# Kernel optimization log

Measured on AMD Instinct MI355X. Metric: run time of the kernel, lower is better.

## Reference

```python
import jax, jax.numpy as jnp
import numpy as np

EPS = 1e-5  # torch BatchNorm1d default eps


def _batchnorm(x, gamma, beta):
    # training-mode BatchNorm1d: biased batch statistics over the N dim
    mean = jnp.mean(x, axis=0)
    var = jnp.var(x, axis=0)
    return (x - mean) * jax.lax.rsqrt(var + EPS) * gamma + beta


def setup_inputs() -> dict:
    key = jax.random.key(0)
    ks = jax.random.split(key, 12)
    N_last, N_cur, E, F = 100000, 50000, 500000, 300
    Din = F + 3  # 303: neighbor features concat coord delta
    inp = {
        "last_coors": jax.random.normal(ks[0], (N_last, 3), jnp.float32),
        "last_features": jax.random.normal(ks[1], (N_last, F), jnp.float32),
        "current_coors": jax.random.normal(ks[2], (N_cur, 3), jnp.float32),
        "cur_idx": jax.random.randint(ks[3], (E,), 0, N_cur),
        "last_idx": jax.random.randint(ks[4], (E,), 0, N_last),
        # in_linear: Linear(303,300) + ReLU + BN(300)
        "W1": jax.random.normal(ks[5], (Din, F), jnp.float32) / np.sqrt(Din),
        "b1": jnp.zeros((F,), jnp.float32),
        "g1": jnp.ones((F,), jnp.float32),
        "be1": jnp.zeros((F,), jnp.float32),
        # out_linear: Linear(300,300) + ReLU + BN(300)
        "W2": jax.random.normal(ks[6], (F, F), jnp.float32) / np.sqrt(F),
        "b2": jnp.zeros((F,), jnp.float32),
        "g2": jnp.ones((F,), jnp.float32),
        "be2": jnp.zeros((F,), jnp.float32),
    }
    return inp


def reference(last_coors, last_features, current_coors, cur_idx, last_idx,
              W1, b1, g1, be1, W2, b2, g2, be2):
    N_cur = current_coors.shape[0]
    # gather: neighbor features + (neighbor - center) coordinate deltas -> [E, 303]
    edge_feats = jnp.concatenate(
        [last_features[last_idx], last_coors[last_idx] - current_coors[cur_idx]],
        axis=1)
    # in_linear MLP on edges
    h = _batchnorm(jnp.maximum(edge_feats @ W1 + b1, 0.0), g1, be1)  # [E, 300]
    # scatter-max aggregation to current-level nodes (empty segments -> 0,
    # matching torch_scatter.scatter(..., reduce='max') zero-init behavior)
    agg = jax.ops.segment_max(h, cur_idx, num_segments=N_cur)  # [N_cur, 300]
    agg = jnp.where(jnp.isfinite(agg), agg, 0.0)
    # out_linear MLP on nodes
    out = _batchnorm(jnp.maximum(agg @ W2 + b2, 0.0), g2, be2)
    return out
```

## Files before the change

### kernel.cpp

```cpp
#include <hip/hip_runtime.h>
#include <hip/hip_bf16.h>


#define NPART 64
#define SB 256
#define SEGB 32
#define CHS 256
#define UNR 8

typedef __bf16 bf16_t;
typedef __bf16 bf16x8 __attribute__((ext_vector_type(8)));
typedef float f32x4 __attribute__((ext_vector_type(4)));

__global__ void hist_k(const int* __restrict__ ci, int E, int* __restrict__ hist)
{
    const int e = blockIdx.x * 256 + threadIdx.x;
    if (e < E) atomicAdd(&hist[ci[e]], 1);
}

__global__ void scan_reduce(const int* __restrict__ hist, int nseg, int* __restrict__ bsum)
{
    __shared__ int s[SB];
    const int tid = threadIdx.x;
    const int i = blockIdx.x * SB + tid;
    s[tid] = (i < nseg) ? hist[i] : 0;
    __syncthreads();
    for (int o = SB / 2; o > 0; o >>= 1) {
        if (tid < o) s[tid] += s[tid + o];
        __syncthreads();
    }
    if (tid == 0) bsum[blockIdx.x] = s[0];
}

__global__ void scan_top(int* __restrict__ bsum, int nb)
{
    __shared__ int s[SB];
    const int tid = threadIdx.x;
    const int v = (tid < nb) ? bsum[tid] : 0;
    s[tid] = v;
    __syncthreads();
    for (int o = 1; o < SB; o <<= 1) {
        int x = 0;
        if (tid >= o) x = s[tid - o];
        __syncthreads();
        s[tid] += x;
        __syncthreads();
    }
    if (tid < nb) bsum[tid] = s[tid] - v;
}

__global__ void scan_final(const int* __restrict__ hist, int nseg,
                           const int* __restrict__ bsum, int* __restrict__ cnt)
{
    __shared__ int s[SB];
    const int tid = threadIdx.x;
    const int i = blockIdx.x * SB + tid;
    const int v = (i < nseg) ? hist[i] : 0;
    s[tid] = v;
    __syncthreads();
    for (int o = 1; o < SB; o <<= 1) {
        int x = 0;
        if (tid >= o) x = s[tid - o];
        __syncthreads();
        s[tid] += x;
        __syncthreads();
    }
    if (i < nseg) cnt[i] = s[tid] - v + bsum[blockIdx.x];
}

__global__ void scatter_k(const int* __restrict__ ci, const int* __restrict__ li,
                          int E, int* __restrict__ cnt, int2* __restrict__ sorted)
{
    const int e = blockIdx.x * 256 + threadIdx.x;
    if (e >= E) return;
    const int c = ci[e];
    const int pos = atomicAdd(&cnt[c], 1);
    sorted[pos] = make_int2(li[e], c);
}

__global__ void pack_wt2(const float* __restrict__ W1, const float* __restrict__ W2,
                         bf16_t* __restrict__ WT)
{
    const int idx = blockIdx.x * 256 + threadIdx.x;
    if (idx >= 2 * 384 * 320) return;
    const int w = idx / (384 * 320);
    const int rem = idx - w * (384 * 320);
    const int n = rem / 320, k = rem % 320;
    const float* W = w ? W2 : W1;
    float v = (n < 300 && k < 300) ? W[k * 300 + n] : 0.f;
    WT[idx] = (bf16_t)v;
}

template<int MODE>
__launch_bounds__(256, 4)
__global__ void gemm_mfma(const float* __restrict__ A32, int M,
                          const int* __restrict__ segEnd,
                          const float* __restrict__ ac,
                          const bf16_t* __restrict__ WT,
                          const float* __restrict__ bias,
                          bf16_t* __restrict__ outBF,
                          float* __restrict__ outF,
                          float* __restrict__ part)
{
    __shared__ bf16_t As[128][72];
    __shared__ float sSum[160], sSq[160];

    const int tid  = threadIdx.x;
    const int lane = tid & 63, wv = tid >> 6;
    const int wm = wv & 1, wn = wv >> 1;
    const int m0 = blockIdx.y * 128, n0 = blockIdx.x * 160;
    const int rl = lane & 15, quad = lane >> 4;

    if (MODE == 1 && tid < 160) { sSum[tid] = 0.f; sSq[tid] = 0.f; }

    const int kcT = (tid & 7) * 8;
    const int rT  = tid >> 3;
    int grow[4]; bool emp[4];
    #pragma unroll
    for (int i = 0; i < 4; ++i) {
        grow[i] = min(m0 + i * 32 + rT, M - 1);
        emp[i] = false;
        if (MODE == 1)
            emp[i] = segEnd[grow[i]] == (grow[i] ? segEnd[grow[i] - 1] : 0);
    }

    f32x4 acc[4][5];
    #pragma unroll
    for (int i = 0; i < 4; ++i)
        #pragma unroll
        for (int j = 0; j < 5; ++j)
            acc[i][j] = (f32x4){0.f, 0.f, 0.f, 0.f};

    for (int k0 = 0; k0 < 320; k0 += 64) {
        const int c0 = k0 + kcT;

        float4 la[4], lb[4];
        float4 aa, ab, ca, cb;
        if (MODE == 1) {
            aa = *reinterpret_cast<const float4*>(&ac[c0]);
            ab = *reinterpret_cast<const float4*>(&ac[c0 + 4]);
            ca = *reinterpret_cast<const float4*>(&ac[320 + c0]);
            cb = *reinterpret_cast<const float4*>(&ac[320 + c0 + 4]);
        }
        #pragma unroll
        for (int i = 0; i < 4; ++i) {
            la[i] = make_float4(0.f, 0.f, 0.f, 0.f);
            lb[i] = make_float4(0.f, 0.f, 0.f, 0.f);
            if (MODE == 0) {
                if (c0 + 8 <= 300) {
                    la[i] = *reinterpret_cast<const float4*>(&A32[(long)grow[i] * 300 + c0]);
                    lb[i] = *reinterpret_cast<const float4*>(&A32[(long)grow[i] * 300 + c0 + 4]);
                } else if (c0 < 300) {
                    la[i] = *reinterpret_cast<const float4*>(&A32[(long)grow[i] * 300 + c0]);
                }
            } else {
                la[i] = *reinterpret_cast<const float4*>(&A32[(long)grow[i] * 320 + c0]);
                lb[i] = *reinterpret_cast<const float4*>(&A32[(long)grow[i] * 320 + c0 + 4]);
            }
        }
        #pragma unroll
        for (int i = 0; i < 4; ++i) {
            bf16x8 v;
            if (MODE == 0) {
                v = (bf16x8){(bf16_t)la[i].x, (bf16_t)la[i].y, (bf16_t)la[i].z, (bf16_t)la[i].w,
                             (bf16_t)lb[i].x, (bf16_t)lb[i].y, (bf16_t)lb[i].z, (bf16_t)lb[i].w};
            } else {
                const float t0 = emp[i] ? 0.f : fabsf(aa.x) * la[i].x + ca.x;
                const float t1 = emp[i] ? 0.f : fabsf(aa.y) * la[i].y + ca.y;
                const float t2 = emp[i] ? 0.f : fabsf(aa.z) * la[i].z + ca.z;
                const float t3 = emp[i] ? 0.f : fabsf(aa.w) * la[i].w + ca.w;
                const float t4 = emp[i] ? 0.f : fabsf(ab.x) * lb[i].x + cb.x;
                const float t5 = emp[i] ? 0.f : fabsf(ab.y) * lb[i].y + cb.y;
                const float t6 = emp[i] ? 0.f : fabsf(ab.z) * lb[i].z + cb.z;
                const float t7 = emp[i] ? 0.f : fabsf(ab.w) * lb[i].w + cb.w;
                v = (bf16x8){(bf16_t)t0, (bf16_t)t1, (bf16_t)t2, (bf16_t)t3,
                             (bf16_t)t4, (bf16_t)t5, (bf16_t)t6, (bf16_t)t7};
            }
            *reinterpret_cast<bf16x8*>(&As[i * 32 + rT][kcT]) = v;
        }
        __syncthreads();

        #pragma unroll
        for (int kk = 0; kk < 2; ++kk) {
            const int kb = kk * 32 + quad * 8;
            bf16x8 af[4], bfr[5];
            #pragma unroll
            for (int nj = 0; nj < 5; ++nj)
                bfr[nj] = *reinterpret_cast<const bf16x8*>(
                    &WT[(long)(n0 + wn * 80 + nj * 16 + rl) * 320 + k0 + kb]);
            #pragma unroll
            for (int mi = 0; mi < 4; ++mi)
                af[mi] = *reinterpret_cast<const bf16x8*>(&As[wm * 64 + mi * 16 + rl][kb]);
            #pragma unroll
            for (int mi = 0; mi < 4; ++mi)
                #pragma unroll
                for (int nj = 0; nj < 5; ++nj)
                    acc[mi][nj] = __builtin_amdgcn_mfma_f32_16x16x32_bf16(
                        af[mi], bfr[nj], acc[mi][nj], 0, 0, 0);
        }
        __syncthreads();
    }

    if (MODE == 0) {
        #pragma unroll
        for (int mi = 0; mi < 4; ++mi)
            #pragma unroll
            for (int nj = 0; nj < 5; ++nj)
                #pragma unroll
                for (int reg = 0; reg < 4; ++reg) {
                    const int r = m0 + wm * 64 + mi * 16 + quad * 4 + reg;
                    const int c = n0 + wn * 80 + nj * 16 + rl;
                    if (r < M) {
                        const float v = (c < 300) ? (acc[mi][nj][reg] + bias[c]) : 0.f;
                        outBF[(long)r * 320 + c] = (bf16_t)v;
                    }
                }
    } else {
        float csum[5] = {}, csq[5] = {};
        #pragma unroll
        for (int mi = 0; mi < 4; ++mi)
            #pragma unroll
            for (int nj = 0; nj < 5; ++nj)
                #pragma unroll
                for (int reg = 0; reg < 4; ++reg) {
                    const int r = m0 + wm * 64 + mi * 16 + quad * 4 + reg;
                    const int c = n0 + wn * 80 + nj * 16 + rl;
                    if (r < M && c < 300) {
                        float v = fmaxf(acc[mi][nj][reg] + bias[c], 0.f);
                        outF[(long)r * 300 + c] = v;
                        csum[nj] += v; csq[nj] += v * v;
                    }
                }
        #pragma unroll
        for (int nj = 0; nj < 5; ++nj) {
            const int cl = wn * 80 + nj * 16 + rl;
            atomicAdd(&sSum[cl], csum[nj]);
            atomicAdd(&sSq[cl], csq[nj]);
        }
        __syncthreads();
        const int slot = (blockIdx.x + blockIdx.y * gridDim.x) & (NPART - 1);
        if (tid < 160 && (n0 + tid) < 300) {
            atomicAdd(&part[slot * 600 + n0 + tid], sSum[tid]);
            atomicAdd(&part[slot * 600 + 300 + n0 + tid], sSq[tid]);
        }
    }
}

__launch_bounds__(320)
__global__ void edge_pass(const bf16_t* __restrict__ Gb,
                          const float* __restrict__ last_coors,
                          const float* __restrict__ cur_coors,
                          const int2* __restrict__ sorted,
                          const int*  __restrict__ segEnd,
                          const float* __restrict__ Wc,
                          const float* __restrict__ g1,
                          float* __restrict__ zbuf,
                          float* __restrict__ part1,
                          int N_cur)
{
    __shared__ int sRow[2][CHS], sCi[2][CHS];
    __shared__ float sD0[2][CHS], sD1[2][CHS], sD2[2][CHS];

    const int tid = threadIdx.x;
    const int st  = (tid >= 160) ? 1 : 0;
    const int ts  = tid - st * 160;

    const int g0   = blockIdx.x * SEGB;
    const int gEnd = min(g0 + SEGB, N_cur);
    const int gMid = min(g0 + SEGB / 2, gEnd);

    const int e00 = (g0   == 0) ? 0 : segEnd[g0 - 1];
    const int e01 = (gMid == 0) ? 0 : segEnd[gMid - 1];
    const int e11 = (gEnd == 0) ? 0 : segEnd[gEnd - 1];

    const int ebeg = st ? e01 : e00;
    const int eend = st ? e11 : e01;

    const int nch0 = (e01 - e00 + CHS - 1) / CHS;
    const int nch1 = (e11 - e01 + CHS - 1) / CHS;
    const int nch  = max(nch0, nch1);

    const int ft = ts * 2;
    const bool real = (ft < 300);
    float w00 = 0.f, w01 = 0.f, w10 = 0.f, w11 = 0.f, w20 = 0.f, w21 = 0.f;
    float sgn0 = 1.f, sgn1 = 1.f;
    if (real) {
        w00 = Wc[ft];        w01 = Wc[ft + 1];
        w10 = Wc[300 + ft];  w11 = Wc[300 + ft + 1];
        w20 = Wc[600 + ft];  w21 = Wc[600 + ft + 1];
        sgn0 = (g1[ft]     < 0.f) ? -1.f : 1.f;
        sgn1 = (g1[ft + 1] < 0.f) ? -1.f : 1.f;
    }

    int cur = -1;
    float m0 = -3.4e38f, m1 = -3.4e38f;
    float sum0 = 0.f, sq0 = 0.f, sum1 = 0.f, sq1 = 0.f;

    for (int ch = 0; ch < nch; ++ch) {
        const int cbeg = ebeg + ch * CHS;
        const int ccnt = min(CHS, eend - cbeg);

        for (int i = ts; i < ccnt; i += 160) {
            const int2 r = sorted[cbeg + i];
            sRow[st][i] = r.x * 320;
            sCi[st][i]  = r.y;
            sD0[st][i] = last_coors[r.x * 3 + 0] - cur_coors[r.y * 3 + 0];
            sD1[st][i] = last_coors[r.x * 3 + 1] - cur_coors[r.y * 3 + 1];
            sD2[st][i] = last_coors[r.x * 3 + 2] - cur_coors[r.y * 3 + 2];
        }
        __syncthreads();

        int i = 0;
        for (; i + UNR <= ccnt; i += UNR) {
            unsigned gu[UNR];
            #pragma unroll
            for (int j = 0; j < UNR; ++j)
                gu[j] = *reinterpret_cast<const unsigned*>(&Gb[(long)sRow[st][i + j] + ft]);
            #pragma unroll
            for (int j = 0; j < UNR; ++j) {
                const int ci = sCi[st][i + j];
                if (ci != cur) {
                    if (cur >= 0)
                        *reinterpret_cast<float2*>(&zbuf[(long)cur * 320 + ft]) =
                            make_float2(m0, m1);
                    cur = ci;
                    m0 = -3.4e38f; m1 = -3.4e38f;
                }
                const float gx = __uint_as_float(gu[j] << 16);
                const float gy = __uint_as_float(gu[j] & 0xffff0000u);
                const float d0 = sD0[st][i + j], d1 = sD1[st][i + j], d2 = sD2[st][i + j];
                const float y0 = fmaxf(gx + d0 * w00 + d1 * w10 + d2 * w20, 0.f);
                const float y1 = fmaxf(gy + d0 * w01 + d1 * w11 + d2 * w21, 0.f);
                sum0 += y0; sq0 += y0 * y0; m0 = fmaxf(m0, sgn0 * y0);
                sum1 += y1; sq1 += y1 * y1; m1 = fmaxf(m1, sgn1 * y1);
            }
        }
        for (; i < ccnt; ++i) {
            const int ci = sCi[st][i];
            if (ci != cur) {
                if (cur >= 0)
                    *reinterpret_cast<float2*>(&zbuf[(long)cur * 320 + ft]) =
                        make_float2(m0, m1);
                cur = ci;
                m0 = -3.4e38f; m1 = -3.4e38f;
            }
            const unsigned gu = *reinterpret_cast<const unsigned*>(&Gb[(long)sRow[st][i] + ft]);
            const float gx = __uint_as_float(gu << 16);
            const float gy = __uint_as_float(gu & 0xffff0000u);
            const float d0 = sD0[st][i], d1 = sD1[st][i], d2 = sD2[st][i];
            const float y0 = fmaxf(gx + d0 * w00 + d1 * w10 + d2 * w20, 0.f);
            const float y1 = fmaxf(gy + d0 * w01 + d1 * w11 + d2 * w21, 0.f);
            sum0 += y0; sq0 += y0 * y0; m0 = fmaxf(m0, sgn0 * y0);
            sum1 += y1; sq1 += y1 * y1; m1 = fmaxf(m1, sgn1 * y1);
        }
        __syncthreads();
    }
    if (cur >= 0)
        *reinterpret_cast<float2*>(&zbuf[(long)cur * 320 + ft]) = make_float2(m0, m1);

    const int slot = blockIdx.x & (NPART - 1);
    if (real) {
        atomicAdd(&part1[slot * 600 + ft],           sum0);
        atomicAdd(&part1[slot * 600 + ft + 1],       sum1);
        atomicAdd(&part1[slot * 600 + 300 + ft],     sq0);
        atomicAdd(&part1[slot * 600 + 300 + ft + 1], sq1);
    }
}

__global__ void stats_finalize(const float* __restrict__ part,
                               const float* __restrict__ g,
                               const float* __restrict__ be,
                               float invCnt, float* __restrict__ ac)
{
    const int t = threadIdx.x;
    if (t >= 300) {
        if (t < 320) { ac[t] = 0.f; ac[320 + t] = 0.f; }
        return;
    }
    float sum = 0.f, sq = 0.f;
    for (int p = 0; p < NPART; ++p) {
        sum += part[p * 600 + t];
        sq  += part[p * 600 + 300 + t];
    }
    const float mean = sum * invCnt;
    const float var = fmaxf(sq * invCnt - mean * mean, 0.f);
    const float inv = rsqrtf(var + 1e-5f);
    const float a = g[t] * inv;
    ac[t] = a;
    ac[320 + t] = be[t] - mean * a;
}

__global__ void finalize_out(float* __restrict__ out,
                             const float* __restrict__ ac2)
{
    const int t = threadIdx.x;
    if (t >= 300) return;
    const long i = (long)blockIdx.x * 300 + t;
    out[i] = ac2[t] * out[i] + ac2[320 + t];
}

extern "C" void kernel_launch(void* const* d_in, const int* in_sizes, int n_in,
                              void* d_out, int out_size, void* d_ws, size_t ws_size,
                              hipStream_t stream)
{
    const float* last_coors    = (const float*)d_in[0];
    const float* last_features = (const float*)d_in[1];
    const float* cur_coors     = (const float*)d_in[2];
    const int*   cur_idx       = (const int*)d_in[3];
    const int*   last_idx      = (const int*)d_in[4];
    const float* W1  = (const float*)d_in[5];
    const float* b1  = (const float*)d_in[6];
    const float* g1  = (const float*)d_in[7];
    const float* be1 = (const float*)d_in[8];
    const float* W2  = (const float*)d_in[9];
    const float* b2  = (const float*)d_in[10];
    const float* g2  = (const float*)d_in[11];
    const float* be2 = (const float*)d_in[12];
    float* out = (float*)d_out;

    const int N_last = in_sizes[0] / 3;
    const int N_cur  = in_sizes[2] / 3;
    const int E      = in_sizes[3];

    const int nb1 = (N_cur + SB - 1) / SB;

    char* ws = (char*)d_ws;
    size_t off = 0;
    bf16_t* Gb = (bf16_t*)(ws + off);  off += (size_t)N_last * 320 * 2;
    off = (off + 255) & ~(size_t)255;
    float* zbuf = (float*)(ws + off);  off += (size_t)N_cur * 320 * 4;
    off = (off + 255) & ~(size_t)255;
    int2* sorted = (int2*)(ws + off);  off += (size_t)E * 8;
    int* hist = (int*)(ws + off);      off += (size_t)nb1 * SB * 4;
    int* cnt  = (int*)(ws + off);      off += (size_t)nb1 * SB * 4;
    int* bsum = (int*)(ws + off);      off += 256 * 4;
    bf16_t* WT1 = (bf16_t*)(ws + off); off += (size_t)384 * 320 * 2;
    bf16_t* WT2 = (bf16_t*)(ws + off); off += (size_t)384 * 320 * 2;
    float* part1 = (float*)(ws + off); off += (size_t)NPART * 600 * 4;
    float* part2 = (float*)(ws + off); off += (size_t)NPART * 600 * 4;
    float* ac1   = (float*)(ws + off); off += 640 * 4;
    float* ac2   = (float*)(ws + off); off += 640 * 4;

    hipMemsetAsync(hist, 0, (size_t)nb1 * SB * 4, stream);
    hipMemsetAsync(part1, 0, (size_t)2 * NPART * 600 * 4, stream);

    hist_k<<<(E + 255) / 256, 256, 0, stream>>>(cur_idx, E, hist);
    scan_reduce<<<nb1, SB, 0, stream>>>(hist, N_cur, bsum);
    scan_top<<<1, SB, 0, stream>>>(bsum, nb1);
    scan_final<<<nb1, SB, 0, stream>>>(hist, N_cur, bsum, cnt);
    scatter_k<<<(E + 255) / 256, 256, 0, stream>>>(cur_idx, last_idx, E, cnt, sorted);

    pack_wt2<<<960, 256, 0, stream>>>(W1, W2, WT1);

    dim3 gridG(2, (N_last + 127) / 128);
    gemm_mfma<0><<<gridG, 256, 0, stream>>>(last_features, N_last, nullptr, nullptr,
                                            WT1, b1, Gb, nullptr, nullptr);

    const int nSB = (N_cur + SEGB - 1) / SEGB;
    edge_pass<<<nSB, 320, 0, stream>>>(Gb, last_coors, cur_coors, sorted, cnt,
                                       W1 + 300 * 300, g1, zbuf, part1, N_cur);

    stats_finalize<<<1, 320, 0, stream>>>(part1, g1, be1, 1.0f / (float)E, ac1);

    dim3 grid2(2, (N_cur + 127) / 128);
    gemm_mfma<1><<<grid2, 256, 0, stream>>>(zbuf, N_cur, cnt, ac1,
                                            WT2, b2, nullptr, out, part2);

    stats_finalize<<<1, 320, 0, stream>>>(part2, g2, be2, 1.0f / (float)N_cur, ac2);
    finalize_out<<<N_cur, 320, 0, stream>>>(out, ac2);
}
```

Baseline: 626.7 us.

## Widen GEMM tiles to full N with 512 threads and stage weights in LDS

The MFMA GEMM kernel now launches 512-thread blocks that each cover all 320 output columns for a 128-row tile, instead of splitting N across two blocks. The A tile is therefore loaded and converted once rather than twice. The weight slice for each K step is now staged cooperatively into shared memory instead of each wave reading it from global memory. In mode 1 the BN scale/shift vector is cached in LDS. The cost is more LDS per block (a 320x72 bf16 B tile plus larger stat arrays) and a larger block, which may reduce the number of blocks resident per CU.

Result: faster. 548.2 us (-12.5%).

```diff
diff --git a/kernel.cpp b/kernel.cpp
--- a/kernel.cpp
+++ b/kernel.cpp
@@ -92,7 +92,7 @@
 }
 
 template<int MODE>
-__launch_bounds__(256, 4)
+__launch_bounds__(512, 4)
 __global__ void gemm_mfma(const float* __restrict__ A32, int M,
                           const int* __restrict__ segEnd,
                           const float* __restrict__ ac,
@@ -103,25 +103,30 @@
                           float* __restrict__ part)
 {
     __shared__ bf16_t As[128][72];
-    __shared__ float sSum[160], sSq[160];
+    __shared__ bf16_t Bs[320][72];
+    __shared__ float sSum[320], sSq[320];
+    __shared__ float sAc[640];
 
     const int tid  = threadIdx.x;
     const int lane = tid & 63, wv = tid >> 6;
     const int wm = wv & 1, wn = wv >> 1;
-    const int m0 = blockIdx.y * 128, n0 = blockIdx.x * 160;
+    const int m0 = blockIdx.x * 128;
     const int rl = lane & 15, quad = lane >> 4;
 
-    if (MODE == 1 && tid < 160) { sSum[tid] = 0.f; sSq[tid] = 0.f; }
+    if (MODE == 1) {
+        if (tid < 320) { sSum[tid] = 0.f; sSq[tid] = 0.f; }
+        for (int i = tid; i < 640; i += 512) sAc[i] = ac[i];
+    }
 
     const int kcT = (tid & 7) * 8;
     const int rT  = tid >> 3;
-    int grow[4]; bool emp[4];
+    int growA[2]; bool emp[2];
     #pragma unroll
-    for (int i = 0; i < 4; ++i) {
-        grow[i] = min(m0 + i * 32 + rT, M - 1);
+    for (int i = 0; i < 2; ++i) {
+        growA[i] = min(m0 + i * 64 + rT, M - 1);
         emp[i] = false;
         if (MODE == 1)
-            emp[i] = segEnd[grow[i]] == (grow[i] ? segEnd[grow[i] - 1] : 0);
+            emp[i] = segEnd[growA[i]] == (growA[i] ? segEnd[growA[i] - 1] : 0);
     }
 
     f32x4 acc[4][5];
@@ -131,40 +136,44 @@
         for (int j = 0; j < 5; ++j)
             acc[i][j] = (f32x4){0.f, 0.f, 0.f, 0.f};
 
+    if (MODE == 1) __syncthreads();
+
     for (int k0 = 0; k0 < 320; k0 += 64) {
         const int c0 = k0 + kcT;
 
-        float4 la[4], lb[4];
-        float4 aa, ab, ca, cb;
-        if (MODE == 1) {
-            aa = *reinterpret_cast<const float4*>(&ac[c0]);
-            ab = *reinterpret_cast<const float4*>(&ac[c0 + 4]);
-            ca = *reinterpret_cast<const float4*>(&ac[320 + c0]);
-            cb = *reinterpret_cast<const float4*>(&ac[320 + c0 + 4]);
-        }
-        #pragma unroll
-        for (int i = 0; i < 4; ++i) {
+        float4 la[2], lb[2];
+        #pragma unroll
+        for (int i = 0; i < 2; ++i) {
             la[i] = make_float4(0.f, 0.f, 0.f, 0.f);
             lb[i] = make_float4(0.f, 0.f, 0.f, 0.f);
             if (MODE == 0) {
                 if (c0 + 8 <= 300) {
-                    la[i] = *reinterpret_cast<const float4*>(&A32[(long)grow[i] * 300 + c0]);
-                    lb[i] = *reinterpret_cast<const float4*>(&A32[(long)grow[i] * 300 + c0 + 4]);
+                    la[i] = *reinterpret_cast<const float4*>(&A32[(long)growA[i] * 300 + c0]);
+                    lb[i] = *reinterpret_cast<const float4*>(&A32[(long)growA[i] * 300 + c0 + 4]);
                 } else if (c0 < 300) {
-                    la[i] = *reinterpret_cast<const float4*>(&A32[(long)grow[i] * 300 + c0]);
+                    la[i] = *reinterpret_cast<const float4*>(&A32[(long)growA[i] * 300 + c0]);
                 }
             } else {
-                la[i] = *reinterpret_cast<const float4*>(&A32[(long)grow[i] * 320 + c0]);
-                lb[i] = *reinterpret_cast<const float4*>(&A32[(long)grow[i] * 320 + c0 + 4]);
+                la[i] = *reinterpret_cast<const float4*>(&A32[(long)growA[i] * 320 + c0]);
+                lb[i] = *reinterpret_cast<const float4*>(&A32[(long)growA[i] * 320 + c0 + 4]);
             }
         }
-        #pragma unroll
-        for (int i = 0; i < 4; ++i) {
+        bf16x8 wb[5];
+        #pragma unroll
+        for (int i = 0; i < 5; ++i)
+            wb[i] = *reinterpret_cast<const bf16x8*>(&WT[(long)(i * 64 + rT) * 320 + c0]);
+
+        #pragma unroll
+        for (int i = 0; i < 2; ++i) {
             bf16x8 v;
             if (MODE == 0) {
                 v = (bf16x8){(bf16_t)la[i].x, (bf16_t)la[i].y, (bf16_t)la[i].z, (bf16_t)la[i].w,
                              (bf16_t)lb[i].x, (bf16_t)lb[i].y, (bf16_t)lb[i].z, (bf16_t)lb[i].w};
             } else {
+                const float4 aa = *reinterpret_cast<const float4*>(&sAc[c0]);
+                const float4 ab = *reinterpret_cast<const float4*>(&sAc[c0 + 4]);
+                const float4 ca = *reinterpret_cast<const float4*>(&sAc[320 + c0]);
+                const float4 cb = *reinterpret_cast<const float4*>(&sAc[320 + c0 + 4]);
                 const float t0 = emp[i] ? 0.f : fabsf(aa.x) * la[i].x + ca.x;
                 const float t1 = emp[i] ? 0.f : fabsf(aa.y) * la[i].y + ca.y;
                 const float t2 = emp[i] ? 0.f : fabsf(aa.z) * la[i].z + ca.z;
@@ -176,8 +185,11 @@
                 v = (bf16x8){(bf16_t)t0, (bf16_t)t1, (bf16_t)t2, (bf16_t)t3,
                              (bf16_t)t4, (bf16_t)t5, (bf16_t)t6, (bf16_t)t7};
             }
-            *reinterpret_cast<bf16x8*>(&As[i * 32 + rT][kcT]) = v;
-        }
+            *reinterpret_cast<bf16x8*>(&As[i * 64 + rT][kcT]) = v;
+        }
+        #pragma unroll
+        for (int i = 0; i < 5; ++i)
+            *reinterpret_cast<bf16x8*>(&Bs[i * 64 + rT][kcT]) = wb[i];
         __syncthreads();
 
         #pragma unroll
@@ -185,12 +197,11 @@
             const int kb = kk * 32 + quad * 8;
             bf16x8 af[4], bfr[5];
             #pragma unroll
-            for (int nj = 0; nj < 5; ++nj)
-                bfr[nj] = *reinterpret_cast<const bf16x8*>(
-                    &WT[(long)(n0 + wn * 80 + nj * 16 + rl) * 320 + k0 + kb]);
-            #pragma unroll
             for (int mi = 0; mi < 4; ++mi)
                 af[mi] = *reinterpret_cast<const bf16x8*>(&As[wm * 64 + mi * 16 + rl][kb]);
+            #pragma unroll
+            for (int nj = 0; nj < 5; ++nj)
+                bfr[nj] = *reinterpret_cast<const bf16x8*>(&Bs[wn * 80 + nj * 16 + rl][kb]);
             #pragma unroll
             for (int mi = 0; mi < 4; ++mi)
                 #pragma unroll
@@ -209,7 +220,7 @@
                 #pragma unroll
                 for (int reg = 0; reg < 4; ++reg) {
                     const int r = m0 + wm * 64 + mi * 16 + quad * 4 + reg;
-                    const int c = n0 + wn * 80 + nj * 16 + rl;
+                    const int c = wn * 80 + nj * 16 + rl;
                     if (r < M) {
                         const float v = (c < 300) ? (acc[mi][nj][reg] + bias[c]) : 0.f;
                         outBF[(long)r * 320 + c] = (bf16_t)v;
@@ -224,7 +235,7 @@
                 #pragma unroll
                 for (int reg = 0; reg < 4; ++reg) {
                     const int r = m0 + wm * 64 + mi * 16 + quad * 4 + reg;
-                    const int c = n0 + wn * 80 + nj * 16 + rl;
+                    const int c = wn * 80 + nj * 16 + rl;
                     if (r < M && c < 300) {
                         float v = fmaxf(acc[mi][nj][reg] + bias[c], 0.f);
                         outF[(long)r * 300 + c] = v;
@@ -234,14 +245,16 @@
         #pragma unroll
         for (int nj = 0; nj < 5; ++nj) {
             const int cl = wn * 80 + nj * 16 + rl;
-            atomicAdd(&sSum[cl], csum[nj]);
-            atomicAdd(&sSq[cl], csq[nj]);
-        }
-        __syncthreads();
-        const int slot = (blockIdx.x + blockIdx.y * gridDim.x) & (NPART - 1);
-        if (tid < 160 && (n0 + tid) < 300) {
-            atomicAdd(&part[slot * 600 + n0 + tid], sSum[tid]);
-            atomicAdd(&part[slot * 600 + 300 + n0 + tid], sSq[tid]);
+            if (cl < 300) {
+                atomicAdd(&sSum[cl], csum[nj]);
+                atomicAdd(&sSq[cl], csq[nj]);
+            }
+        }
+        __syncthreads();
+        const int slot = blockIdx.x & (NPART - 1);
+        if (tid < 300) {
+            atomicAdd(&part[slot * 600 + tid], sSum[tid]);
+            atomicAdd(&part[slot * 600 + 300 + tid], sSq[tid]);
         }
     }
 }
@@ -452,9 +465,8 @@
 
     pack_wt2<<<960, 256, 0, stream>>>(W1, W2, WT1);
 
-    dim3 gridG(2, (N_last + 127) / 128);
-    gemm_mfma<0><<<gridG, 256, 0, stream>>>(last_features, N_last, nullptr, nullptr,
-                                            WT1, b1, Gb, nullptr, nullptr);
+    gemm_mfma<0><<<(N_last + 127) / 128, 512, 0, stream>>>(
+        last_features, N_last, nullptr, nullptr, WT1, b1, Gb, nullptr, nullptr);
 
     const int nSB = (N_cur + SEGB - 1) / SEGB;
     edge_pass<<<nSB, 320, 0, stream>>>(Gb, last_coors, cur_coors, sorted, cnt,
@@ -462,9 +474,8 @@
 
     stats_finalize<<<1, 320, 0, stream>>>(part1, g1, be1, 1.0f / (float)E, ac1);
 
-    dim3 grid2(2, (N_cur + 127) / 128);
-    gemm_mfma<1><<<grid2, 256, 0, stream>>>(zbuf, N_cur, cnt, ac1,
-                                            WT2, b2, nullptr, out, part2);
+    gemm_mfma<1><<<(N_cur + 127) / 128, 512, 0, stream>>>(
+        zbuf, N_cur, cnt, ac1, WT2, b2, nullptr, out, part2);
 
     stats_finalize<<<1, 320, 0, stream>>>(part2, g2, be2, 1.0f / (float)N_cur, ac2);
     finalize_out<<<N_cur, 320, 0, stream>>>(out, ac2);
```
